# Kernel tuning notes

Measured on AMD Instinct MI355X. Metric: run time of the kernel, lower is better.

## Reference

```python
import jax, jax.numpy as jnp
import numpy as np

B, CIN, COUT, H, KS = 16, 64, 64, 224, 7


def setup_inputs() -> dict:
    key = jax.random.key(0)
    k1, k2 = jax.random.split(key)
    x = jax.random.normal(k1, (B, CIN, H, H), dtype=jnp.float32)
    # kaiming_uniform_ default (a=0, fan_in mode): bound = sqrt(6 / fan_in)
    fan_in = CIN * KS * KS
    bound = float(np.sqrt(6.0 / fan_in))
    kernel = jax.random.uniform(k2, (COUT, CIN, KS, KS), minval=-bound, maxval=bound, dtype=jnp.float32)
    return {"input": x, "kernel": kernel}


def _kernel_spectrum(k2d, n):
    # Pad kernel to the optical plane size (n x n), centered, then ifftshift so the
    # frequency-domain product implements a centered circular convolution (4f system).
    ks = k2d.shape[-1]
    s = (n - ks) // 2
    pad = jnp.zeros(k2d.shape[:-2] + (n, n), k2d.dtype)
    pad = pad.at[..., s:s + ks, s:s + ks].set(k2d)
    return jnp.fft.fft2(jnp.fft.ifftshift(pad, axes=(-2, -1)))


def reference(input, kernel):
    n = input.shape[-1]
    # Original loop bug: in_channel index is always 0, so
    # out[b,oc] = optConv2d(sum_ic input[b,ic], kernel[oc,0])
    kf = _kernel_spectrum(kernel[:, 0], n)          # [O, H, W] complex
    sf = jnp.fft.fft2(input.sum(axis=1))            # [B, H, W] complex
    out = jnp.fft.ifft2(sf[:, None] * kf[None]).real  # [B, O, H, W]
    return out.astype(input.dtype)
```

## Files before the change

### kernel.cpp

```cpp
#include <hip/hip_runtime.h>
#include <hip/hip_bf16.h>

#define Hn 224
#define HWn (224*224)
#define B_ 16
#define CIN_ 64
#define COUT_ 64
#define PR 230
#define PC 240
#define PHW (PR*PC)
#define GUARD 1024

typedef __attribute__((ext_vector_type(4)))  float f32x4;
typedef __attribute__((ext_vector_type(8)))  short bf16x8;
typedef __attribute__((ext_vector_type(16))) float f32x16;

__global__ __launch_bounds__(256) void chan_sum_kernel(const float* __restrict__ x,
                                                       float* __restrict__ Sp) {
    int idx = blockIdx.x * 256 + threadIdx.x;
    const int npix4 = B_ * HWn / 4;
    if (idx >= npix4) return;
    const int s4 = HWn / 4;
    int b  = idx / s4;
    int p4 = idx - b * s4;
    const f32x4* xb = (const f32x4*)x + (size_t)b * CIN_ * s4 + p4;

    f32x4 a0 = __builtin_nontemporal_load(xb + 0 * s4);
    f32x4 a1 = __builtin_nontemporal_load(xb + 1 * s4);
    f32x4 a2 = __builtin_nontemporal_load(xb + 2 * s4);
    f32x4 a3 = __builtin_nontemporal_load(xb + 3 * s4);
    #pragma unroll 4
    for (int c = 4; c < CIN_; c += 4) {
        a0 += __builtin_nontemporal_load(xb + (size_t)(c + 0) * s4);
        a1 += __builtin_nontemporal_load(xb + (size_t)(c + 1) * s4);
        a2 += __builtin_nontemporal_load(xb + (size_t)(c + 2) * s4);
        a3 += __builtin_nontemporal_load(xb + (size_t)(c + 3) * s4);
    }
    f32x4 r = (a0 + a1) + (a2 + a3);
    float v0 = r.x, v1 = r.y, v2 = r.z, v3 = r.w;

    int y  = p4 / 56;
    int x0 = (p4 - y * 56) * 4;
    float* Sb = Sp + (size_t)b * PHW;

    float* dst = Sb + (size_t)(y + 2) * PC + 2 + x0;
    dst[0] = v0; dst[1] = v1; dst[2] = v2; dst[3] = v3;

    if (y < 4) {
        float* d = Sb + (size_t)(y + 226) * PC + 2 + x0;
        d[0] = v0; d[1] = v1; d[2] = v2; d[3] = v3;
    }
    if (y >= 222) {
        float* d = Sb + (size_t)(y - 222) * PC + 2 + x0;
        d[0] = v0; d[1] = v1; d[2] = v2; d[3] = v3;
    }
    if (x0 == 0) {
        float* d = Sb + (size_t)(y + 2) * PC + 226;
        d[0] = v0; d[1] = v1; d[2] = v2; d[3] = v3;
        if (y < 4) {
            float* e = Sb + (size_t)(y + 226) * PC + 226;
            e[0] = v0; e[1] = v1; e[2] = v2; e[3] = v3;
        }
        if (y >= 222) {
            float* e = Sb + (size_t)(y - 222) * PC + 226;
            e[0] = v0; e[1] = v1; e[2] = v2; e[3] = v3;
        }
    }
    if (x0 == 220) {
        float* d = Sb + (size_t)(y + 2) * PC;
        d[0] = v2; d[1] = v3;
        if (y < 4) {
            float* e = Sb + (size_t)(y + 226) * PC;
            e[0] = v2; e[1] = v3;
        }
        if (y >= 222) {
            float* e = Sb + (size_t)(y - 222) * PC;
            e[0] = v2; e[1] = v3;
        }
    }
}

__global__ __launch_bounds__(128, 4) void conv_mfma(const float* __restrict__ Sp,
                                                    const float* __restrict__ K,
                                                    float* __restrict__ out) {
    const int yg = blockIdx.x;
    const int b  = blockIdx.y;
    const int wv = threadIdx.x >> 6;
    const int l  = threadIdx.x & 63;
    const int y   = yg * 2 + wv;
    const int lo5 = l & 31;
    const int hi  = l >> 5;

    bf16x8 afrag[2][4];
    #pragma unroll
    for (int g = 0; g < 2; ++g) {
        const int m = g * 32 + lo5;
        #pragma unroll
        for (int c = 0; c < 4; ++c) {
            const int ky = 2 * c + hi;
            const float* kp = K + (size_t)m * (CIN_ * 49) + ky * 7;
            const bool ok = (ky < 7);
            float f0 = ok ? kp[0] : 0.f, f1 = ok ? kp[1] : 0.f;
            float f2 = ok ? kp[2] : 0.f, f3 = ok ? kp[3] : 0.f;
            float f4 = ok ? kp[4] : 0.f, f5 = ok ? kp[5] : 0.f;
            float f6 = ok ? kp[6] : 0.f, f7 = 0.f;
            union { int i[4]; bf16x8 v; } au;
            asm("v_cvt_pk_bf16_f32 %0, %1, %2" : "=v"(au.i[0]) : "v"(f0), "v"(f1));
            asm("v_cvt_pk_bf16_f32 %0, %1, %2" : "=v"(au.i[1]) : "v"(f2), "v"(f3));
            asm("v_cvt_pk_bf16_f32 %0, %1, %2" : "=v"(au.i[2]) : "v"(f4), "v"(f5));
            asm("v_cvt_pk_bf16_f32 %0, %1, %2" : "=v"(au.i[3]) : "v"(f6), "v"(f7));
            afrag[g][c] = au.v;
        }
    }

    const float* Sb = Sp + (size_t)b * PHW;
    float* outb = out + (size_t)b * COUT_ * HWn + (size_t)y * Hn;

    for (int xt = 0; xt < 7; ++xt) {
        const int x0 = xt * 32;

        f32x16 acc0, acc1;
        #pragma unroll
        for (int i = 0; i < 16; ++i) { acc0[i] = 0.0f; acc1[i] = 0.0f; }

        #pragma unroll
        for (int c = 0; c < 4; ++c) {
            const int rowg = y + 6 - (2 * c + hi);
            const float* rp = Sb + rowg * PC + x0 + 6 + lo5;
            union { int i[4]; bf16x8 v; } bu;
            #pragma unroll
            for (int j = 0; j < 4; ++j) {
                float flo = rp[-(2 * j)];
                float fhi = rp[-(2 * j) - 1];
                asm("v_cvt_pk_bf16_f32 %0, %1, %2" : "=v"(bu.i[j]) : "v"(flo), "v"(fhi));
            }
            acc0 = __builtin_amdgcn_mfma_f32_32x32x16_bf16(afrag[0][c], bu.v, acc0, 0, 0, 0);
            acc1 = __builtin_amdgcn_mfma_f32_32x32x16_bf16(afrag[1][c], bu.v, acc1, 0, 0, 0);
        }

        #pragma unroll
        for (int r = 0; r < 16; ++r) {
            const int row = (r & 3) + 8 * (r >> 2) + 4 * hi;
            outb[(size_t)row        * HWn + x0 + lo5] = acc0[r];
            outb[(size_t)(32 + row) * HWn + x0 + lo5] = acc1[r];
        }
    }
}

extern "C" void kernel_launch(void* const* d_in, const int* in_sizes, int n_in,
                              void* d_out, int out_size, void* d_ws, size_t ws_size,
                              hipStream_t stream) {
    const float* x = (const float*)d_in[0];
    const float* K = (const float*)d_in[1];
    float* out = (float*)d_out;
    float* Sp = (float*)d_ws + GUARD;

    const int npix4 = B_ * HWn / 4;
    chan_sum_kernel<<<(npix4 + 255) / 256, 256, 0, stream>>>(x, Sp);

    dim3 g2(112, 16);
    conv_mfma<<<g2, 128, 0, stream>>>(Sp, K, out);
}
```

Measured before the change: 84.21 us.

## Fuse channel-sum and conv into persistent kernel with per-batch readiness counters

Replaces the two separate launches with a persistent fused kernel. Workgroups first pull channel-sum work items from an atomic queue, then pull conv work items, spin-waiting on a per-batch completion counter so conv for one batch can overlap the channel sum of later batches. Weight bf16 conversion moves to a small prep kernel so conv items load packed fragments directly. This adds a memset and an extra launch, halves the occupancy hint, and adds spin-wait and atomic overhead, and the spin has a timeout escape that could read incomplete data.

```diff
diff --git a/kernel.cpp b/kernel.cpp
--- a/kernel.cpp
+++ b/kernel.cpp
@@ -10,20 +10,31 @@
 #define PC 240
 #define PHW (PR*PC)
 #define GUARD 1024
+#define WOFF  (4*1024*1024)
+#define CTROFF (8*1024*1024)
+#define NK1   1792
+#define NCONV 1792
+#define DONE_TGT 112
 
 typedef __attribute__((ext_vector_type(4)))  float f32x4;
 typedef __attribute__((ext_vector_type(8)))  short bf16x8;
 typedef __attribute__((ext_vector_type(16))) float f32x16;
 
-__global__ __launch_bounds__(256) void chan_sum_kernel(const float* __restrict__ x,
-                                                       float* __restrict__ Sp) {
-    int idx = blockIdx.x * 256 + threadIdx.x;
-    const int npix4 = B_ * HWn / 4;
-    if (idx >= npix4) return;
+__global__ __launch_bounds__(256) void wprep_kernel(const float* __restrict__ K,
+                                                    unsigned short* __restrict__ W) {
+    int i = blockIdx.x * 256 + threadIdx.x;
+    if (i >= 64 * 64) return;
+    int oc = i >> 6, kk = i & 63;
+    int ky = kk >> 3, kx = kk & 7;
+    float v = (ky < 7 && kx < 7) ? K[(size_t)oc * (CIN_ * 49) + ky * 7 + kx] : 0.0f;
+    __hip_bfloat16 h = __float2bfloat16(v);
+    W[i] = *(unsigned short*)&h;
+}
+
+__device__ __forceinline__ void k1_unit(const float* __restrict__ x,
+                                        float* __restrict__ Sb, int b, int y, int q) {
     const int s4 = HWn / 4;
-    int b  = idx / s4;
-    int p4 = idx - b * s4;
-    const f32x4* xb = (const f32x4*)x + (size_t)b * CIN_ * s4 + p4;
+    const f32x4* xb = (const f32x4*)x + (size_t)b * CIN_ * s4 + (y * 56 + q);
 
     f32x4 a0 = __builtin_nontemporal_load(xb + 0 * s4);
     f32x4 a1 = __builtin_nontemporal_load(xb + 1 * s4);
@@ -38,10 +49,7 @@
     }
     f32x4 r = (a0 + a1) + (a2 + a3);
     float v0 = r.x, v1 = r.y, v2 = r.z, v3 = r.w;
-
-    int y  = p4 / 56;
-    int x0 = (p4 - y * 56) * 4;
-    float* Sb = Sp + (size_t)b * PHW;
+    const int x0 = q * 4;
 
     float* dst = Sb + (size_t)(y + 2) * PC + 2 + x0;
     dst[0] = v0; dst[1] = v1; dst[2] = v2; dst[3] = v3;
@@ -80,11 +88,9 @@
     }
 }
 
-__global__ __launch_bounds__(128, 4) void conv_mfma(const float* __restrict__ Sp,
-                                                    const float* __restrict__ K,
-                                                    float* __restrict__ out) {
-    const int yg = blockIdx.x;
-    const int b  = blockIdx.y;
+__device__ __forceinline__ void conv_item(const float* __restrict__ Sp,
+                                          const unsigned short* __restrict__ W,
+                                          float* __restrict__ out, int b, int yg) {
     const int wv = threadIdx.x >> 6;
     const int l  = threadIdx.x & 63;
     const int y   = yg * 2 + wv;
@@ -93,32 +99,16 @@
 
     bf16x8 afrag[2][4];
     #pragma unroll
-    for (int g = 0; g < 2; ++g) {
-        const int m = g * 32 + lo5;
-        #pragma unroll
-        for (int c = 0; c < 4; ++c) {
-            const int ky = 2 * c + hi;
-            const float* kp = K + (size_t)m * (CIN_ * 49) + ky * 7;
-            const bool ok = (ky < 7);
-            float f0 = ok ? kp[0] : 0.f, f1 = ok ? kp[1] : 0.f;
-            float f2 = ok ? kp[2] : 0.f, f3 = ok ? kp[3] : 0.f;
-            float f4 = ok ? kp[4] : 0.f, f5 = ok ? kp[5] : 0.f;
-            float f6 = ok ? kp[6] : 0.f, f7 = 0.f;
-            union { int i[4]; bf16x8 v; } au;
-            asm("v_cvt_pk_bf16_f32 %0, %1, %2" : "=v"(au.i[0]) : "v"(f0), "v"(f1));
-            asm("v_cvt_pk_bf16_f32 %0, %1, %2" : "=v"(au.i[1]) : "v"(f2), "v"(f3));
-            asm("v_cvt_pk_bf16_f32 %0, %1, %2" : "=v"(au.i[2]) : "v"(f4), "v"(f5));
-            asm("v_cvt_pk_bf16_f32 %0, %1, %2" : "=v"(au.i[3]) : "v"(f6), "v"(f7));
-            afrag[g][c] = au.v;
-        }
-    }
+    for (int g = 0; g < 2; ++g)
+        #pragma unroll
+        for (int c = 0; c < 4; ++c)
+            afrag[g][c] = *(const bf16x8*)(W + ((g * 32 + lo5) * 64 + c * 16 + hi * 8));
 
     const float* Sb = Sp + (size_t)b * PHW;
     float* outb = out + (size_t)b * COUT_ * HWn + (size_t)y * Hn;
 
     for (int xt = 0; xt < 7; ++xt) {
         const int x0 = xt * 32;
-
         f32x16 acc0, acc1;
         #pragma unroll
         for (int i = 0; i < 16; ++i) { acc0[i] = 0.0f; acc1[i] = 0.0f; }
@@ -147,6 +137,53 @@
     }
 }
 
+__global__ __launch_bounds__(128, 2) void fused_kernel(const float* __restrict__ x,
+                                                       const unsigned short* __restrict__ W,
+                                                       float* __restrict__ Sp,
+                                                       float* __restrict__ out,
+                                                       int* __restrict__ ctrs) {
+    __shared__ int sI;
+    int* k1c   = ctrs + 0;
+    int* convc = ctrs + 1;
+    int* done  = ctrs + 2;
+
+    for (;;) {
+        __syncthreads();
+        if (threadIdx.x == 0) sI = atomicAdd(k1c, 1);
+        __syncthreads();
+        int i = sI;
+        if (i >= NK1) break;
+        int b = i / 112, r = i - b * 112;
+        float* Sb = Sp + (size_t)b * PHW;
+        int t = threadIdx.x;
+        if (t < 112) k1_unit(x, Sb, b, r * 2 + t / 56, t % 56);
+        __syncthreads();
+        if (threadIdx.x == 0) {
+            __threadfence();
+            __hip_atomic_fetch_add(&done[b], 1, __ATOMIC_RELEASE, __HIP_MEMORY_SCOPE_AGENT);
+        }
+    }
+
+    for (;;) {
+        __syncthreads();
+        if (threadIdx.x == 0) sI = atomicAdd(convc, 1);
+        __syncthreads();
+        int j = sI;
+        if (j >= NCONV) break;
+        int b = j / 112, yg = j - b * 112;
+        if (threadIdx.x == 0) {
+            int spin = 0;
+            while (__hip_atomic_load(&done[b], __ATOMIC_ACQUIRE,
+                                     __HIP_MEMORY_SCOPE_AGENT) < DONE_TGT) {
+                __builtin_amdgcn_s_sleep(8);
+                if (++spin > 2000000) break;
+            }
+        }
+        __syncthreads();
+        conv_item(Sp, W, out, b, yg);
+    }
+}
+
 extern "C" void kernel_launch(void* const* d_in, const int* in_sizes, int n_in,
                               void* d_out, int out_size, void* d_ws, size_t ws_size,
                               hipStream_t stream) {
@@ -154,10 +191,10 @@
     const float* K = (const float*)d_in[1];
     float* out = (float*)d_out;
     float* Sp = (float*)d_ws + GUARD;
-
-    const int npix4 = B_ * HWn / 4;
-    chan_sum_kernel<<<(npix4 + 255) / 256, 256, 0, stream>>>(x, Sp);
-
-    dim3 g2(112, 16);
-    conv_mfma<<<g2, 128, 0, stream>>>(Sp, K, out);
-}
+    unsigned short* W = (unsigned short*)((char*)d_ws + WOFF);
+    int* ctrs = (int*)((char*)d_ws + CTROFF);
+
+    hipMemsetAsync(ctrs, 0, 256, stream);
+    wprep_kernel<<<16, 256, 0, stream>>>(K, W);
+    fused_kernel<<<1024, 128, 0, stream>>>(x, W, Sp, out, ctrs);
+}
```

Measured after the change: 286.4 us. 3.4x slower.
